# Kernel tuning notes

Measured on AMD Instinct MI355X. Metric: run time of the kernel, lower is better.

The kernel has to match this reference:

```python
import jax, jax.numpy as jnp
import numpy as np

# module constants (match init_kwargs)
D_MODEL = 1024
N_HEADS = 16
D_K = 64
CHUNK_LEN = 64
EPS = 1e-8

B, C, N, NL = 4, 16, 2, 128  # batch, chunks, neighbors, neighbor_len
S = C * CHUNK_LEN            # seq_len = 1024


def setup_inputs() -> dict:
    key = jax.random.key(0)
    ks = jax.random.split(key, 10)
    s = 0.02
    HD = N_HEADS * D_K
    return {
        "h": jax.random.normal(ks[0], (B, S, D_MODEL), jnp.float32),
        "e": jax.random.normal(ks[1], (B, C, N, NL, D_MODEL), jnp.float32),
        "g_norm": jnp.ones((D_MODEL,), jnp.float32),
        "Wq": jax.random.normal(ks[2], (D_MODEL, HD), jnp.float32) * s,
        "bq": jnp.zeros((HD,), jnp.float32),
        "Wk": jax.random.normal(ks[3], (D_MODEL, HD), jnp.float32) * s,
        "bk": jnp.zeros((HD,), jnp.float32),
        "Wv": jax.random.normal(ks[4], (D_MODEL, HD), jnp.float32) * s,
        "bv": jnp.zeros((HD,), jnp.float32),
        "Wo": jax.random.normal(ks[5], (HD, D_MODEL), jnp.float32) * s,
        "bo": jnp.zeros((D_MODEL,), jnp.float32),
    }


def _rmsnorm(x, g):
    return x * g * jax.lax.rsqrt(jnp.mean(x * x, axis=-1, keepdims=True) + EPS)


def reference(h, e, g_norm, Wq, bq, Wk, bk, Wv, bv, Wo, bo):
    b, seq, d = h.shape
    _, c, n, nl, _ = e.shape
    cl = CHUNK_LEN
    scale = 1.0 / np.sqrt(D_K).astype(np.float32)

    h_res = h
    hn = _rmsnorm(h[:, cl - 1:], g_norm)                 # [b, seq-cl+1, d]
    pad = c * cl - hn.shape[1]
    hn = jnp.pad(hn, ((0, 0), (0, pad), (0, 0)))         # [b, c*cl, d]
    hn = hn.reshape(b, c, cl, d)

    q = (hn @ Wq + bq).reshape(b, c, cl, N_HEADS, D_K)       # bcihd
    k = (e @ Wk + bk).reshape(b, c, n, nl, N_HEADS, D_K)     # bcnjhd
    v = (e @ Wv + bv).reshape(b, c, n, nl, N_HEADS, D_K)

    attn = jnp.einsum('bcihd,bcnjhd->bchinj', q, k) * scale  # [b,c,h,i,n,j]
    attn = jax.nn.softmax(attn.reshape(b, c, N_HEADS, cl, n * nl), axis=-1)
    attn = attn.reshape(b, c, N_HEADS, cl, n, nl)

    o = jnp.einsum('bchinj,bcnjhd->bcihd', attn, v)
    o = o.reshape(b, c * cl, N_HEADS * D_K)
    o = o @ Wo + bo                                          # [b, c*cl, d]
    o = jnp.pad(o, ((0, 0), (cl - 1, 0), (0, 0)))            # shift right by cl-1
    return o[:, :seq] + h_res
```

## Files before the change

### kernel.cpp

```cpp
#include <hip/hip_runtime.h>
#include <stdint.h>

#define DEV __device__ __forceinline__

typedef __attribute__((ext_vector_type(8))) __bf16 bf16x8;
typedef __attribute__((ext_vector_type(4))) float floatx4;

DEV unsigned int f2bf(float f) {
  union { float f; unsigned int i; } x; x.f = f;
  unsigned int r = x.i + 0x7FFFu + ((x.i >> 16) & 1u);
  return r >> 16;
}
DEV void gl2lds16(const unsigned short* g, unsigned short* l) {
  __builtin_amdgcn_global_load_lds(
      (const __attribute__((address_space(1))) unsigned int*)g,
      (__attribute__((address_space(3))) unsigned int*)l, 16, 0, 0);
}
DEV floatx4 zero4() { floatx4 z; z[0]=0.f; z[1]=0.f; z[2]=0.f; z[3]=0.f; return z; }

__global__ void cca_prep_k(const float* __restrict__ W0, const float* __restrict__ W1,
                           const float* __restrict__ W2, const float* __restrict__ W3,
                           unsigned short* __restrict__ D0, unsigned short* __restrict__ D1,
                           unsigned short* __restrict__ D2, unsigned short* __restrict__ D3,
                           const float* __restrict__ e, unsigned short* __restrict__ eb,
                           const float* __restrict__ h, const float* __restrict__ g,
                           unsigned short* __restrict__ hn, float* __restrict__ out) {
  __shared__ float tile[64][65];
  int blk = blockIdx.x;
  int t = threadIdx.x;
  if (blk < 1024) {
    const float* W; unsigned short* Wt;
    switch (blk >> 8) {
      case 0: W = W0; Wt = D0; break;
      case 1: W = W1; Wt = D1; break;
      case 2: W = W2; Wt = D2; break;
      default: W = W3; Wt = D3; break;
    }
    int k0 = (blk & 15) * 64, n0 = ((blk >> 4) & 15) * 64;
    int c = t & 63, r4 = t >> 6;
#pragma unroll
    for (int it = 0; it < 16; ++it) {
      int r = it * 4 + r4;
      tile[r][c] = W[(size_t)(k0 + r) * 1024 + n0 + c];
    }
    __syncthreads();
#pragma unroll
    for (int it = 0; it < 16; ++it) {
      int r = it * 4 + r4;
      Wt[(size_t)(n0 + r) * 1024 + k0 + c] = (unsigned short)f2bf(tile[c][r]);
    }
    return;
  }
  if (blk < 17408) {
    int i = (blk - 1024) * 256 + t;
    float4 v = ((const float4*)e)[i];
    uint2 o;
    o.x = f2bf(v.x) | (f2bf(v.y) << 16);
    o.y = f2bf(v.z) | (f2bf(v.w) << 16);
    ((uint2*)eb)[i] = o;
    return;
  }
  if (blk < 21504) {
    int row = blk - 17408;
    int b = row >> 10, p = row & 1023;
    unsigned short* dst = hn + (size_t)row * 1024;
    if (p >= 961) {
      uint2 z; z.x = 0u; z.y = 0u;
      ((uint2*)dst)[t] = z;
      return;
    }
    const float* src = h + ((size_t)(b << 10) + p + 63) * 1024;
    float4 v = ((const float4*)src)[t];
    float ss = v.x*v.x + v.y*v.y + v.z*v.z + v.w*v.w;
#pragma unroll
    for (int m = 32; m > 0; m >>= 1) ss += __shfl_down(ss, m);
    __shared__ float wsum[4];
    int lane = t & 63, wv = t >> 6;
    if (lane == 0) wsum[wv] = ss;
    __syncthreads();
    float tot = wsum[0] + wsum[1] + wsum[2] + wsum[3];
    float r = rsqrtf(tot * (1.0f / 1024.0f) + 1e-8f);
    float4 gv = ((const float4*)g)[t];
    uint2 outp;
    outp.x = f2bf(v.x * gv.x * r) | (f2bf(v.y * gv.y * r) << 16);
    outp.y = f2bf(v.z * gv.z * r) | (f2bf(v.w * gv.w * r) << 16);
    ((uint2*)dst)[t] = outp;
    return;
  }
  {
    int idx = (blk - 21504) * 256 + t;
    const int n4 = 4 * 63 * 1024 / 4;
    if (idx < n4) {
      int e4 = idx * 4;
      int b = e4 / (63 * 1024);
      int r = e4 - b * (63 * 1024);
      size_t off = (size_t)b * 1024 * 1024 + (size_t)r;
      *(float4*)(out + off) = *(const float4*)(h + off);
    }
  }
}

__launch_bounds__(256, 2)
__global__ void cca_gemmQKV_k(const unsigned short* __restrict__ eb,
                              const unsigned short* __restrict__ WkvT,
                              const float* __restrict__ bk,
                              const float* __restrict__ bv,
                              unsigned short* __restrict__ KVb,
                              const unsigned short* __restrict__ hn,
                              const unsigned short* __restrict__ WqT,
                              const float* __restrict__ bq,
                              unsigned short* __restrict__ Qb) {
  __shared__ unsigned short Ash[128 * 64];
  __shared__ unsigned short Bsh[128 * 64];
  int blk = blockIdx.x;
  const unsigned short *A, *Bt;
  int tM, tN;
  bool isQ = (blk >= 2048), isV = false;
  if (!isQ) {
    int mblk = blk >> 4, n = blk & 15;
    tM = mblk * 128; tN = n * 128; isV = (n >= 8);
    A = eb; Bt = WkvT;
  } else {
    int q = blk - 2048;
    tM = (q >> 3) * 128; tN = (q & 7) * 128;
    A = hn; Bt = WqT;
  }
  int t = threadIdx.x, lane = t & 63, wv = t >> 6;
  int wm = wv >> 1, wn = wv & 1;
  int l15 = lane & 15, quad = lane >> 4;
  int arow = lane >> 3, achk = lane & 7;
  int gchk = achk ^ arow;
  floatx4 acc[4][4];
#pragma unroll
  for (int i = 0; i < 4; ++i)
#pragma unroll
    for (int j = 0; j < 4; ++j) acc[i][j] = zero4();

  for (int k0 = 0; k0 < 1024; k0 += 64) {
    __syncthreads();
#pragma unroll
    for (int ii = 0; ii < 4; ++ii) {
      int seg = ii * 4 + wv;
      int row = seg * 8 + arow;
      gl2lds16(A + (size_t)(tM + row) * 1024 + k0 + gchk * 8, Ash + seg * 512);
      gl2lds16(Bt + (size_t)(tN + row) * 1024 + k0 + gchk * 8, Bsh + seg * 512);
    }
    __syncthreads();
#pragma unroll
    for (int hseg = 0; hseg < 2; ++hseg) {
      int u = (hseg << 2) | quad;
      bf16x8 af[4], bfv[4];
#pragma unroll
      for (int mt = 0; mt < 4; ++mt) {
        int r = wm * 64 + mt * 16 + l15;
        af[mt] = *(const bf16x8*)&Ash[r * 64 + ((u ^ (l15 & 7)) << 3)];
      }
#pragma unroll
      for (int nt = 0; nt < 4; ++nt) {
        int r = wn * 64 + nt * 16 + l15;
        bfv[nt] = *(const bf16x8*)&Bsh[r * 64 + ((u ^ (l15 & 7)) << 3)];
      }
#pragma unroll
      for (int mt = 0; mt < 4; ++mt)
#pragma unroll
        for (int nt = 0; nt < 4; ++nt)
          acc[mt][nt] = __builtin_amdgcn_mfma_f32_16x16x32_bf16(af[mt], bfv[nt], acc[mt][nt], 0, 0, 0);
    }
  }

  if (isV) {
    int chunk = tM >> 8;
    int keybase = tM & 255;
    unsigned short* vdst = KVb + (size_t)chunk * 524288 + 1024;
#pragma unroll
    for (int mt = 0; mt < 4; ++mt) {
      int key = keybase + wm * 64 + mt * 16 + quad * 4;
      int u = key >> 3, j0 = key & 7;
#pragma unroll
      for (int nt = 0; nt < 4; ++nt) {
        int dcol = (tN - 1024) + wn * 64 + nt * 16 + l15;
        int hh = dcol >> 6, d = dcol & 63;
        float bs = bv[dcol];
        uint2 o;
        o.x = f2bf(acc[mt][nt][0] + bs) | (f2bf(acc[mt][nt][1] + bs) << 16);
        o.y = f2bf(acc[mt][nt][2] + bs) | (f2bf(acc[mt][nt][3] + bs) << 16);
        int idx = d * 256 + ((u ^ (d & 7)) << 3) + j0;
        *(uint2*)(vdst + (size_t)(hh * 16 + (idx >> 10)) * 2048 + (idx & 1023)) = o;
      }
    }
    return;
  }
#pragma unroll
  for (int mt = 0; mt < 4; ++mt) {
    int mrow = tM + wm * 64 + mt * 16 + quad * 4;
#pragma unroll
    for (int nt = 0; nt < 4; ++nt) {
      int ncol = tN + wn * 64 + nt * 16 + l15;
      float bs = isQ ? bq[ncol] : bk[ncol];
#pragma unroll
      for (int r = 0; r < 4; ++r) {
        int m = mrow + r;
        if (isQ) Qb[(size_t)m * 1024 + ncol] = (unsigned short)f2bf(acc[mt][nt][r] + bs);
        else     KVb[(size_t)m * 2048 + ncol] = (unsigned short)f2bf(acc[mt][nt][r] + bs);
      }
    }
  }
}

__launch_bounds__(256, 2)
__global__ void cca_gemmO_k(const unsigned short* __restrict__ A,
                            const unsigned short* __restrict__ Bt,
                            const float* __restrict__ bias,
                            const float* __restrict__ resid,
                            float* __restrict__ out) {
  __shared__ unsigned short Ash[128 * 64];
  __shared__ unsigned short Bsh[64 * 64];
  int tM = blockIdx.x * 128, tN = blockIdx.y * 64;
  int t = threadIdx.x, lane = t & 63, wv = t >> 6;
  int wm = wv >> 1, wn = wv & 1;
  int l15 = lane & 15, quad = lane >> 4;
  int arow = lane >> 3, achk = lane & 7;
  int gchk = achk ^ arow;
  floatx4 acc[4][2];
#pragma unroll
  for (int i = 0; i < 4; ++i)
#pragma unroll
    for (int j = 0; j < 2; ++j) acc[i][j] = zero4();

  for (int k0 = 0; k0 < 1024; k0 += 64) {
    __syncthreads();
#pragma unroll
    for (int ii = 0; ii < 4; ++ii) {
      int seg = ii * 4 + wv;
      int row = seg * 8 + arow;
      gl2lds16(A + (size_t)(tM + row) * 1024 + k0 + gchk * 8, Ash + seg * 512);
    }
#pragma unroll
    for (int ii = 0; ii < 2; ++ii) {
      int seg = ii * 4 + wv;
      int row = seg * 8 + arow;
      gl2lds16(Bt + (size_t)(tN + row) * 1024 + k0 + gchk * 8, Bsh + seg * 512);
    }
    __syncthreads();
#pragma unroll
    for (int hseg = 0; hseg < 2; ++hseg) {
      int u = (hseg << 2) | quad;
      bf16x8 af[4], bfv[2];
#pragma unroll
      for (int mt = 0; mt < 4; ++mt) {
        int r = wm * 64 + mt * 16 + l15;
        af[mt] = *(const bf16x8*)&Ash[r * 64 + ((u ^ (l15 & 7)) << 3)];
      }
#pragma unroll
      for (int nt = 0; nt < 2; ++nt) {
        int r = wn * 32 + nt * 16 + l15;
        bfv[nt] = *(const bf16x8*)&Bsh[r * 64 + ((u ^ (l15 & 7)) << 3)];
      }
#pragma unroll
      for (int mt = 0; mt < 4; ++mt)
#pragma unroll
        for (int nt = 0; nt < 2; ++nt)
          acc[mt][nt] = __builtin_amdgcn_mfma_f32_16x16x32_bf16(af[mt], bfv[nt], acc[mt][nt], 0, 0, 0);
    }
  }

#pragma unroll
  for (int mt = 0; mt < 4; ++mt) {
    int mrow = tM + wm * 64 + mt * 16 + quad * 4;
#pragma unroll
    for (int nt = 0; nt < 2; ++nt) {
      int ncol = tN + wn * 32 + nt * 16 + l15;
      float bs = bias[ncol];
#pragma unroll
      for (int r = 0; r < 4; ++r) {
        int m = mrow + r;
        int p = m & 1023;
        if (p < 961) {
          size_t o = (size_t)(m + 63) * 1024 + (size_t)ncol;
          out[o] = acc[mt][nt][r] + bs + resid[o];
        }
      }
    }
  }
}

__launch_bounds__(256, 2)
__global__ void cca_attn_k(const unsigned short* __restrict__ Q,
                           const unsigned short* __restrict__ KV,
                           unsigned short* __restrict__ O) {
  __shared__ unsigned short smemA[64 * 64 + 256 * 64];
  __shared__ unsigned short VTlds[64 * 256];
  unsigned short* Qsh = smemA;
  unsigned short* Ksh = smemA + 64 * 64;
  unsigned short* Psh = smemA;
  int bch = blockIdx.x;
  int hh = bch & 15, c = (bch >> 4) & 15, b = bch >> 8;
  int t = threadIdx.x, lane = t & 63, wv = t >> 6;
  int l15 = lane & 15, quad = lane >> 4;
  size_t qbase = (size_t)b * 1024 + (size_t)c * 64;
  size_t kvbase = (size_t)b * 4096 + (size_t)c * 256;
  int hoff = hh * 64;

  {
    int rowi = lane >> 3, chk = lane & 7;
#pragma unroll
    for (int ii = 0; ii < 2; ++ii) {
      int seg = wv + ii * 4;
      int row = seg * 8 + rowi;
      gl2lds16(Q + (qbase + row) * 1024 + hoff + chk * 8, Qsh + seg * 512);
    }
#pragma unroll
    for (int ii = 0; ii < 8; ++ii) {
      int seg = wv + ii * 4;
      int row = seg * 8 + rowi;
      gl2lds16(KV + (kvbase + row) * 2048 + hoff + chk * 8, Ksh + seg * 512);
    }
    const unsigned short* vbase = KV + (size_t)(b * 16 + c) * 524288 + 1024;
#pragma unroll
    for (int ii = 0; ii < 8; ++ii) {
      int seg = wv + ii * 4;
      int i = seg * 512 + lane * 8;
      gl2lds16(vbase + (size_t)(hh * 16 + (i >> 10)) * 2048 + (i & 1023),
               VTlds + seg * 512);
    }
  }
  __syncthreads();

  floatx4 st[16];
#pragma unroll
  for (int i = 0; i < 16; ++i) st[i] = zero4();
  bf16x8 a0 = *(const bf16x8*)&Qsh[(wv * 16 + l15) * 64 + quad * 8];
  bf16x8 a1 = *(const bf16x8*)&Qsh[(wv * 16 + l15) * 64 + 32 + quad * 8];
#pragma unroll
  for (int kt = 0; kt < 16; ++kt) {
    bf16x8 b0 = *(const bf16x8*)&Ksh[(kt * 16 + l15) * 64 + quad * 8];
    bf16x8 b1 = *(const bf16x8*)&Ksh[(kt * 16 + l15) * 64 + 32 + quad * 8];
    st[kt] = __builtin_amdgcn_mfma_f32_16x16x32_bf16(a0, b0, st[kt], 0, 0, 0);
    st[kt] = __builtin_amdgcn_mfma_f32_16x16x32_bf16(a1, b1, st[kt], 0, 0, 0);
  }
  __syncthreads();

  const float scale = 0.125f;
#pragma unroll
  for (int r = 0; r < 4; ++r) {
    float mx = -1e30f;
#pragma unroll
    for (int kt = 0; kt < 16; ++kt) mx = fmaxf(mx, st[kt][r]);
    mx = fmaxf(mx, __shfl_xor(mx, 1));
    mx = fmaxf(mx, __shfl_xor(mx, 2));
    mx = fmaxf(mx, __shfl_xor(mx, 4));
    mx = fmaxf(mx, __shfl_xor(mx, 8));
    float sum = 0.f;
#pragma unroll
    for (int kt = 0; kt < 16; ++kt) {
      float e = __expf((st[kt][r] - mx) * scale);
      st[kt][r] = e;
      sum += e;
    }
    sum += __shfl_xor(sum, 1);
    sum += __shfl_xor(sum, 2);
    sum += __shfl_xor(sum, 4);
    sum += __shfl_xor(sum, 8);
    float inv = 1.0f / sum;
    int prow = wv * 16 + quad * 4 + r;
#pragma unroll
    for (int kt = 0; kt < 16; ++kt)
      Psh[prow * 264 + kt * 16 + l15] = (unsigned short)f2bf(st[kt][r] * inv);
  }

  floatx4 ot[4];
#pragma unroll
  for (int nt = 0; nt < 4; ++nt) ot[nt] = zero4();
#pragma unroll
  for (int kt2 = 0; kt2 < 8; ++kt2) {
    bf16x8 ap = *(const bf16x8*)&Psh[(wv * 16 + l15) * 264 + kt2 * 32 + quad * 8];
#pragma unroll
    for (int nt = 0; nt < 4; ++nt) {
      int vrow = nt * 16 + l15;
      int u = kt2 * 4 + quad;
      bf16x8 bv8 = *(const bf16x8*)&VTlds[vrow * 256 + ((u ^ (vrow & 7)) << 3)];
      ot[nt] = __builtin_amdgcn_mfma_f32_16x16x32_bf16(ap, bv8, ot[nt], 0, 0, 0);
    }
  }
#pragma unroll
  for (int nt = 0; nt < 4; ++nt) {
#pragma unroll
    for (int r = 0; r < 4; ++r) {
      int i = wv * 16 + quad * 4 + r;
      int dcol = hoff + nt * 16 + l15;
      O[(qbase + i) * 1024 + dcol] = (unsigned short)f2bf(ot[nt][r]);
    }
  }
}

extern "C" void kernel_launch(void* const* d_in, const int* in_sizes, int n_in,
                              void* d_out, int out_size, void* d_ws, size_t ws_size,
                              hipStream_t stream) {
  const float* h  = (const float*)d_in[0];
  const float* e  = (const float*)d_in[1];
  const float* g  = (const float*)d_in[2];
  const float* Wq = (const float*)d_in[3];
  const float* bq = (const float*)d_in[4];
  const float* Wk = (const float*)d_in[5];
  const float* bk = (const float*)d_in[6];
  const float* Wv = (const float*)d_in[7];
  const float* bv = (const float*)d_in[8];
  const float* Wo = (const float*)d_in[9];
  const float* bo = (const float*)d_in[10];
  float* out = (float*)d_out;

  unsigned short* ws   = (unsigned short*)d_ws;
  unsigned short* hn   = ws;
  unsigned short* WqT  = hn   + (size_t)4096 * 1024;
  unsigned short* WkvT = WqT  + (size_t)1024 * 1024;
  unsigned short* WoT  = WkvT + (size_t)2048 * 1024;
  unsigned short* Qb   = WoT  + (size_t)1024 * 1024;
  unsigned short* KVb  = Qb   + (size_t)4096 * 1024;
  unsigned short* Ob   = KVb  + (size_t)16384 * 2048;
  unsigned short* eb   = Ob   + (size_t)4096 * 1024;

  cca_prep_k<<<21756, 256, 0, stream>>>(
      Wq, Wk, Wv, Wo, WqT, WkvT, WkvT + (size_t)1024 * 1024, WoT,
      e, eb, h, g, hn, out);

  cca_gemmQKV_k<<<2304, 256, 0, stream>>>(eb, WkvT, bk, bv, KVb,
                                          hn, WqT, bq, Qb);

  cca_attn_k<<<1024, 256, 0, stream>>>(Qb, KVb, Ob);

  cca_gemmO_k<<<dim3(32, 16), 256, 0, stream>>>(Ob, WoT, bo, h, out);
}
```

Baseline: 281.0 us.

## Stage V-transpose stores through LDS and remap block order for L2 reuse

```diff
diff --git a/kernel.cpp b/kernel.cpp
--- a/kernel.cpp
+++ b/kernel.cpp
@@ -110,19 +110,23 @@
                               const unsigned short* __restrict__ WqT,
                               const float* __restrict__ bq,
                               unsigned short* __restrict__ Qb) {
-  __shared__ unsigned short Ash[128 * 64];
-  __shared__ unsigned short Bsh[128 * 64];
+  __shared__ unsigned short smem[128 * 64 * 2];
+  unsigned short* Ash = smem;
+  unsigned short* Bsh = smem + 128 * 64;
   int blk = blockIdx.x;
   const unsigned short *A, *Bt;
   int tM, tN;
   bool isQ = (blk >= 2048), isV = false;
   if (!isQ) {
-    int mblk = blk >> 4, n = blk & 15;
+    int x = blk & 7, s = blk >> 3;
+    int mblk = x * 16 + (s & 15), n = s >> 4;
     tM = mblk * 128; tN = n * 128; isV = (n >= 8);
     A = eb; Bt = WkvT;
   } else {
     int q = blk - 2048;
-    tM = (q >> 3) * 128; tN = (q & 7) * 128;
+    int x = q & 7, s = q >> 3;
+    int mblk = x * 4 + (s & 3), n = s >> 2;
+    tM = mblk * 128; tN = n * 128;
     A = hn; Bt = WqT;
   }
   int t = threadIdx.x, lane = t & 63, wv = t >> 6;
@@ -171,22 +175,37 @@
   if (isV) {
     int chunk = tM >> 8;
     int keybase = tM & 255;
-    unsigned short* vdst = KVb + (size_t)chunk * 524288 + 1024;
+    int hh0 = (tN - 1024) >> 6;
+    unsigned short* VTsh = smem;
+    __syncthreads();
 #pragma unroll
     for (int mt = 0; mt < 4; ++mt) {
-      int key = keybase + wm * 64 + mt * 16 + quad * 4;
-      int u = key >> 3, j0 = key & 7;
+      int kl = wm * 64 + mt * 16 + quad * 4;
+      int ul = kl >> 3;
+      int j0 = kl & 7;
 #pragma unroll
       for (int nt = 0; nt < 4; ++nt) {
-        int dcol = (tN - 1024) + wn * 64 + nt * 16 + l15;
-        int hh = dcol >> 6, d = dcol & 63;
-        float bs = bv[dcol];
+        int d = nt * 16 + l15;
+        float bs = bv[(tN - 1024) + wn * 64 + d];
+        int off = (wn * 64 + d) * 128 + ((ul ^ (d & 7)) << 3) + j0;
         uint2 o;
         o.x = f2bf(acc[mt][nt][0] + bs) | (f2bf(acc[mt][nt][1] + bs) << 16);
         o.y = f2bf(acc[mt][nt][2] + bs) | (f2bf(acc[mt][nt][3] + bs) << 16);
-        int idx = d * 256 + ((u ^ (d & 7)) << 3) + j0;
-        *(uint2*)(vdst + (size_t)(hh * 16 + (idx >> 10)) * 2048 + (idx & 1023)) = o;
-      }
+        *(uint2*)&VTsh[off] = o;
+      }
+    }
+    __syncthreads();
+    unsigned short* vdst = KVb + (size_t)chunk * 524288 + 1024;
+#pragma unroll
+    for (int it = 0; it < 8; ++it) {
+      int flat = it * 256 + t;
+      int seg = flat >> 4;
+      int u16 = flat & 15;
+      int hhl = seg >> 6, d = seg & 63;
+      int hh = hh0 + hhl;
+      size_t dst = (size_t)(hh * 16 + (d >> 2)) * 2048 +
+                   (d & 3) * 256 + keybase + u16 * 8;
+      *(uint4*)(vdst + dst) = *(const uint4*)&VTsh[seg * 128 + u16 * 8];
     }
     return;
   }
```

Result: faster. 274.3 us (-2.4%).
